# Kernel optimization log

Measured on AMD Instinct MI355X. Metric: run time of the kernel, lower is better.

Reference implementation:

```python
import jax, jax.numpy as jnp
import numpy as np

EPS = 1e-05
SCALING = 1.0


def setup_inputs() -> dict:
    key = jax.random.key(0)
    k0, k1, k2, k3, k4, k5 = jax.random.split(key, 6)
    Nx = Ny = Nz = 160          # output grid resolution per axis
    D = 48                      # factor (Kronecker) rank per axis
    W = 3                       # width0: output channels (3D flow)
    NP = 2_000_000              # query points
    K = 8                       # interpolation taps per point (trilinear)
    x = jax.random.normal(k0, (Nx, D), dtype=jnp.float32)
    y = jax.random.normal(k1, (Ny, D), dtype=jnp.float32)
    z = jax.random.normal(k2, (Nz, D), dtype=jnp.float32)
    # matches torch init: 2/sqrt(W)*rand - 1/sqrt(W)
    weight = (2.0 / np.sqrt(W)) * jax.random.uniform(k3, (W, D, D, D), dtype=jnp.float32) - (1.0 / np.sqrt(W))
    B_idx = jax.random.randint(k4, (NP, K), 0, Nx * Ny * Nz, dtype=jnp.int32)
    B_w = jax.random.uniform(k5, (NP, K), dtype=jnp.float32)
    return {"x": x, "y": y, "z": z, "weight": weight, "B_idx": B_idx, "B_w": B_w}


def reference(x, y, z, weight, B_idx, B_w):
    # Tensor-mode (Kronecker) matmuls: (W,D0,D1,D2) -> (W,Nx,Ny,Nz)
    g = jnp.einsum('ap,wpqr->waqr', x, weight)   # contract mode-0
    g = jnp.einsum('bq,waqr->wabr', y, g)        # contract mode-1
    g = jnp.einsum('cr,wabr->wabc', z, g)        # contract mode-2
    # Total-variation regularizer (isotropic, per-voxel sqrt, channel-summed)
    base = g[:, :-1, :-1, :-1]
    tv = jnp.mean(
        jnp.sqrt(
            EPS
            + (g[:, :-1, :-1, 1:] - base) ** 2
            + (g[:, :-1, 1:, :-1] - base) ** 2
            + (g[:, 1:, :-1, :-1] - base) ** 2
        ).sum(axis=0)
    )
    reg_scaled = tv * SCALING
    # Gather-weighted interpolation: flat grid (Ncells, W), K taps per point
    flat = g.reshape(g.shape[0], -1).T            # (Nx*Ny*Nz, W)
    out = (flat[B_idx] * B_w[..., None]).sum(axis=1)  # (NP, W)
    return out, reg_scaled
```

## Files before the change

### kernel.cpp

```cpp
#include <hip/hip_runtime.h>
#include <hip/hip_fp16.h>

#define D 48
#define W 3
#define NX 160
#define NY 160
#define NZ 160
#define NPTS (NX*NY*NZ)
#define KNBR 8
#define EPSV 1e-5f
#define NTV (159*159*159)
#define NBTV 2048
#define TVROWS (159*159)
#define CPAIRS 80
#define TVSLOTS (TVROWS*CPAIRS)

typedef int   vint4   __attribute__((ext_vector_type(4)));
typedef float vfloat4 __attribute__((ext_vector_type(4)));

#define T1_OFF 0
#define T1_SZ (W*NX*D*D)
#define TVP_OFF (T1_OFF + T1_SZ)
#define G3_OFF (TVP_OFF + NBTV)

__device__ inline void unpack3(uint2 u, float& f0, float& f1, float& f2) {
    __half2 lo = *reinterpret_cast<__half2*>(&u.x);
    __half2 hi = *reinterpret_cast<__half2*>(&u.y);
    f0 = __low2float(lo);
    f1 = __high2float(lo);
    f2 = __low2float(hi);
}

__global__ __launch_bounds__(256) void k1(const float* __restrict__ x,
                                          const float* __restrict__ wt,
                                          float* __restrict__ t1) {
    int lane = threadIdx.x & 63;
    int wv   = threadIdx.x >> 6;
    int q    = blockIdx.x * 4 + wv;
    int a0   = blockIdx.y * 16;
    int w    = blockIdx.z;
    bool act = lane < D;

    float wreg[D];
#pragma unroll
    for (int p = 0; p < D; ++p)
        wreg[p] = act ? wt[((w*D + p)*D + q)*D + lane] : 0.f;

    for (int ai = 0; ai < 16; ++ai) {
        int a = a0 + ai;
        const float4* xp = (const float4*)(x + a*D);
        float s = 0.f;
#pragma unroll
        for (int j = 0; j < D/4; ++j) {
            float4 xv = xp[j];
            s += xv.x * wreg[4*j+0];
            s += xv.y * wreg[4*j+1];
            s += xv.z * wreg[4*j+2];
            s += xv.w * wreg[4*j+3];
        }
        if (act) t1[((w*NX + a)*D + q)*D + lane] = s;
    }
}

#define BH 80
__global__ __launch_bounds__(192) void kbcd(const float* __restrict__ y,
                                            const float* __restrict__ z,
                                            const float* __restrict__ t1,
                                            uint2* __restrict__ g3h) {
    __shared__ float t1s[W*D*D];
    __shared__ float t2s[W*BH*D];
    int tid = threadIdx.x;
    int a   = blockIdx.y;
    int b0  = blockIdx.x * BH;

    int c = tid;
    bool act = c < NZ;
    float zreg[D];
#pragma unroll
    for (int j = 0; j < D/4; ++j) {
        float4 zv = act ? ((const float4*)(z + c*D))[j] : make_float4(0,0,0,0);
        zreg[4*j+0] = zv.x; zreg[4*j+1] = zv.y; zreg[4*j+2] = zv.z; zreg[4*j+3] = zv.w;
    }

    for (int i = tid; i < W*D*D; i += 192) {
        int w = i / (D*D), rem = i - w*(D*D);
        t1s[i] = t1[(size_t)(w*NX + a)*(D*D) + rem];
    }
    __syncthreads();

    for (int i = tid; i < W*BH*(D/4); i += 192) {
        int w   = i / (BH*(D/4));
        int rem = i - w*(BH*(D/4));
        int bh  = rem / (D/4);
        int r4  = rem - bh*(D/4);
        const float4* yb  = (const float4*)(y + (b0 + bh)*D);
        const float4* t1v = (const float4*)(t1s + w*D*D) + r4;
        float4 s = make_float4(0,0,0,0);
#pragma unroll
        for (int q4 = 0; q4 < D/4; ++q4) {
            float4 yv = yb[q4];
#pragma unroll
            for (int u = 0; u < 4; ++u) {
                float yq = (u==0) ? yv.x : (u==1) ? yv.y : (u==2) ? yv.z : yv.w;
                float4 tv = t1v[(q4*4+u)*(D/4)];
                s.x += yq*tv.x; s.y += yq*tv.y; s.z += yq*tv.z; s.w += yq*tv.w;
            }
        }
        ((float4*)t2s)[i] = s;
    }
    __syncthreads();

    for (int bh = 0; bh < BH; ++bh) {
        float acc[W];
#pragma unroll
        for (int w = 0; w < W; ++w) {
            const float4* t2v = (const float4*)(t2s + (w*BH + bh)*D);
            float s = 0.f;
#pragma unroll
            for (int j = 0; j < D/4; ++j) {
                float4 t = t2v[j];
                s += t.x*zreg[4*j+0] + t.y*zreg[4*j+1] + t.z*zreg[4*j+2] + t.w*zreg[4*j+3];
            }
            acc[w] = s;
        }
        if (act) {
            __half2 lo = __halves2half2(__float2half_rn(acc[0]), __float2half_rn(acc[1]));
            __half2 hi = __halves2half2(__float2half_rn(acc[2]), __float2half_rn(0.f));
            uint2 u;
            u.x = *reinterpret_cast<unsigned*>(&lo);
            u.y = *reinterpret_cast<unsigned*>(&hi);
            g3h[(size_t)((a*NY + (b0+bh))*NZ + c)] = u;
        }
    }
}

__device__ inline float tv3(uint2 u0, uint2 uc, uint2 ub, uint2 ua) {
    float b0,b1,b2, c0,c1,c2, d0,d1,d2, e0,e1,e2;
    unpack3(u0,b0,b1,b2); unpack3(uc,c0,c1,c2);
    unpack3(ub,d0,d1,d2); unpack3(ua,e0,e1,e2);
    float x0=c0-b0, y0=d0-b0, z0=e0-b0;
    float x1=c1-b1, y1=d1-b1, z1=e1-b1;
    float x2=c2-b2, y2=d2-b2, z2=e2-b2;
    return sqrtf(EPSV + x0*x0 + y0*y0 + z0*z0)
         + sqrtf(EPSV + x1*x1 + y1*y1 + z1*z1)
         + sqrtf(EPSV + x2*x2 + y2*y2 + z2*z2);
}

__global__ __launch_bounds__(256) void ktv(const uint2* __restrict__ g3h,
                                           float* __restrict__ partial) {
    float v = 0.f;
    for (int s = blockIdx.x * 256 + threadIdx.x; s < TVSLOTS; s += NBTV * 256) {
        int c2  = s % CPAIRS;
        int row = s / CPAIRS;
        int b   = row % 159;
        int a   = row / 159;
        int c   = 2*c2;
        size_t p = (size_t)(a*NY + b)*NZ + c;
        uint4 u0 = *(const uint4*)(g3h + p);
        uint4 ub = *(const uint4*)(g3h + p + NZ);
        uint4 ua = *(const uint4*)(g3h + p + NY*NZ);
        uint2 un = g3h[p + 2];
        uint2 u0l = make_uint2(u0.x, u0.y), u0h = make_uint2(u0.z, u0.w);
        uint2 ubl = make_uint2(ub.x, ub.y), ubh = make_uint2(ub.z, ub.w);
        uint2 ual = make_uint2(ua.x, ua.y), uah = make_uint2(ua.z, ua.w);
        v += tv3(u0l, u0h, ubl, ual);
        if (c + 1 < 159)
            v += tv3(u0h, un, ubh, uah);
    }
#pragma unroll
    for (int off = 32; off > 0; off >>= 1)
        v += __shfl_down(v, off, 64);
    __shared__ float sred[4];
    int lane = threadIdx.x & 63, wv = threadIdx.x >> 6;
    if (lane == 0) sred[wv] = v;
    __syncthreads();
    if (threadIdx.x == 0)
        partial[blockIdx.x] = sred[0] + sred[1] + sred[2] + sred[3];
}

__global__ __launch_bounds__(256) void kred(const float* __restrict__ partial,
                                            float* __restrict__ outreg) {
    float v = 0.f;
    for (int i = threadIdx.x; i < NBTV; i += 256) v += partial[i];
#pragma unroll
    for (int off = 32; off > 0; off >>= 1)
        v += __shfl_down(v, off, 64);
    __shared__ float sred[4];
    int lane = threadIdx.x & 63, wv = threadIdx.x >> 6;
    if (lane == 0) sred[wv] = v;
    __syncthreads();
    if (threadIdx.x == 0)
        outreg[0] = (sred[0] + sred[1] + sred[2] + sred[3]) * (1.0f / (float)NTV);
}

__global__ __launch_bounds__(256) void kgather(const int* __restrict__ bidx,
                                               const float* __restrict__ bw,
                                               const uint2* __restrict__ g3h,
                                               float* __restrict__ out,
                                               int np) {
    int gid  = blockIdx.x * 256 + threadIdx.x;
    int half = np >> 1;
    if (gid >= half) return;
    int n1 = gid, n2 = gid + half;

    const vint4*   ip = (const vint4*)bidx;
    const vfloat4* wp = (const vfloat4*)bw;
    vint4   i0 = __builtin_nontemporal_load(ip + (size_t)n1*2);
    vint4   i1 = __builtin_nontemporal_load(ip + (size_t)n1*2 + 1);
    vint4   j0 = __builtin_nontemporal_load(ip + (size_t)n2*2);
    vint4   j1 = __builtin_nontemporal_load(ip + (size_t)n2*2 + 1);
    vfloat4 w0 = __builtin_nontemporal_load(wp + (size_t)n1*2);
    vfloat4 w1 = __builtin_nontemporal_load(wp + (size_t)n1*2 + 1);
    vfloat4 v0 = __builtin_nontemporal_load(wp + (size_t)n2*2);
    vfloat4 v1 = __builtin_nontemporal_load(wp + (size_t)n2*2 + 1);

    int   idsA[KNBR] = {i0.x, i0.y, i0.z, i0.w, i1.x, i1.y, i1.z, i1.w};
    int   idsB[KNBR] = {j0.x, j0.y, j0.z, j0.w, j1.x, j1.y, j1.z, j1.w};
    float wwsA[KNBR] = {w0.x, w0.y, w0.z, w0.w, w1.x, w1.y, w1.z, w1.w};
    float wwsB[KNBR] = {v0.x, v0.y, v0.z, v0.w, v1.x, v1.y, v1.z, v1.w};

    uint2 uA[KNBR], uB[KNBR];
#pragma unroll
    for (int k = 0; k < KNBR; ++k) uA[k] = g3h[(size_t)idsA[k]];
#pragma unroll
    for (int k = 0; k < KNBR; ++k) uB[k] = g3h[(size_t)idsB[k]];

    float a0=0.f, a1=0.f, a2=0.f, b0=0.f, b1=0.f, b2=0.f;
#pragma unroll
    for (int k = 0; k < KNBR; ++k) {
        float f0,f1,f2;
        unpack3(uA[k], f0,f1,f2);
        a0 += f0*wwsA[k]; a1 += f1*wwsA[k]; a2 += f2*wwsA[k];
    }
#pragma unroll
    for (int k = 0; k < KNBR; ++k) {
        float f0,f1,f2;
        unpack3(uB[k], f0,f1,f2);
        b0 += f0*wwsB[k]; b1 += f1*wwsB[k]; b2 += f2*wwsB[k];
    }
    float* opA = out + (size_t)n1*3;
    float* opB = out + (size_t)n2*3;
    __builtin_nontemporal_store(a0, opA+0);
    __builtin_nontemporal_store(a1, opA+1);
    __builtin_nontemporal_store(a2, opA+2);
    __builtin_nontemporal_store(b0, opB+0);
    __builtin_nontemporal_store(b1, opB+1);
    __builtin_nontemporal_store(b2, opB+2);
}

extern "C" void kernel_launch(void* const* d_in, const int* in_sizes, int n_in,
                              void* d_out, int out_size, void* d_ws, size_t ws_size,
                              hipStream_t stream) {
    const float* x    = (const float*)d_in[0];
    const float* y    = (const float*)d_in[1];
    const float* z    = (const float*)d_in[2];
    const float* wt   = (const float*)d_in[3];
    const int*   bidx = (const int*)d_in[4];
    const float* bw   = (const float*)d_in[5];
    float* out = (float*)d_out;
    float* ws  = (float*)d_ws;

    float* t1  = ws + T1_OFF;
    float* tvp = ws + TVP_OFF;
    uint2* g3h = (uint2*)(ws + G3_OFF);
    int np = in_sizes[4] / KNBR;

    k1  <<<dim3(12, 10, 3), 256, 0, stream>>>(x, wt, t1);
    kbcd<<<dim3(2, NX),     192, 0, stream>>>(y, z, t1, g3h);

    ktv <<<dim3(NBTV), 256, 0, stream>>>(g3h, tvp);
    kred<<<dim3(1),    256, 0, stream>>>(tvp, out + (out_size - 1));

    kgather<<<dim3((np/2 + 255) / 256), 256, 0, stream>>>(bidx, bw, g3h, out, np);
}
```

Before: 524.3 us.

## Process gather taps in address slices with block sync for cache locality

The gather kernel now handles four points per thread instead of two. It walks the 4M-entry fp16 grid in 16 slices of 2^18 cells, and each thread fetches only the taps whose index falls in the current slice, with a __syncthreads between slices. The aim is to keep all blocks on the GPU working in one region of the grid at a time so the random gathers hit L2 or infinity cache more often. The cost is serialised, divergent loop passes, fewer loads in flight per thread, a barrier per slice, and fewer threads overall. Blocks are not synchronised across the whole GPU, so the locality only holds loosely.

New measurement: 1.705 ms. 3.25x slower.

```diff
diff --git a/kernel.cpp b/kernel.cpp
--- a/kernel.cpp
+++ b/kernel.cpp
@@ -14,6 +14,10 @@
 #define TVROWS (159*159)
 #define CPAIRS 80
 #define TVSLOTS (TVROWS*CPAIRS)
+
+#define SLICES 16
+#define SLICE_SHIFT 18
+#define PPT 4
 
 typedef int   vint4   __attribute__((ext_vector_type(4)));
 typedef float vfloat4 __attribute__((ext_vector_type(4)));
@@ -198,54 +202,59 @@
                                                const uint2* __restrict__ g3h,
                                                float* __restrict__ out,
                                                int np) {
-    int gid  = blockIdx.x * 256 + threadIdx.x;
-    int half = np >> 1;
-    if (gid >= half) return;
-    int n1 = gid, n2 = gid + half;
+    int gid = blockIdx.x * 256 + threadIdx.x;
+    int nth = np / PPT;
+    if (gid >= nth) return;
 
     const vint4*   ip = (const vint4*)bidx;
     const vfloat4* wp = (const vfloat4*)bw;
-    vint4   i0 = __builtin_nontemporal_load(ip + (size_t)n1*2);
-    vint4   i1 = __builtin_nontemporal_load(ip + (size_t)n1*2 + 1);
-    vint4   j0 = __builtin_nontemporal_load(ip + (size_t)n2*2);
-    vint4   j1 = __builtin_nontemporal_load(ip + (size_t)n2*2 + 1);
-    vfloat4 w0 = __builtin_nontemporal_load(wp + (size_t)n1*2);
-    vfloat4 w1 = __builtin_nontemporal_load(wp + (size_t)n1*2 + 1);
-    vfloat4 v0 = __builtin_nontemporal_load(wp + (size_t)n2*2);
-    vfloat4 v1 = __builtin_nontemporal_load(wp + (size_t)n2*2 + 1);
-
-    int   idsA[KNBR] = {i0.x, i0.y, i0.z, i0.w, i1.x, i1.y, i1.z, i1.w};
-    int   idsB[KNBR] = {j0.x, j0.y, j0.z, j0.w, j1.x, j1.y, j1.z, j1.w};
-    float wwsA[KNBR] = {w0.x, w0.y, w0.z, w0.w, w1.x, w1.y, w1.z, w1.w};
-    float wwsB[KNBR] = {v0.x, v0.y, v0.z, v0.w, v1.x, v1.y, v1.z, v1.w};
-
-    uint2 uA[KNBR], uB[KNBR];
-#pragma unroll
-    for (int k = 0; k < KNBR; ++k) uA[k] = g3h[(size_t)idsA[k]];
-#pragma unroll
-    for (int k = 0; k < KNBR; ++k) uB[k] = g3h[(size_t)idsB[k]];
-
-    float a0=0.f, a1=0.f, a2=0.f, b0=0.f, b1=0.f, b2=0.f;
-#pragma unroll
-    for (int k = 0; k < KNBR; ++k) {
-        float f0,f1,f2;
-        unpack3(uA[k], f0,f1,f2);
-        a0 += f0*wwsA[k]; a1 += f1*wwsA[k]; a2 += f2*wwsA[k];
-    }
-#pragma unroll
-    for (int k = 0; k < KNBR; ++k) {
-        float f0,f1,f2;
-        unpack3(uB[k], f0,f1,f2);
-        b0 += f0*wwsB[k]; b1 += f1*wwsB[k]; b2 += f2*wwsB[k];
-    }
-    float* opA = out + (size_t)n1*3;
-    float* opB = out + (size_t)n2*3;
-    __builtin_nontemporal_store(a0, opA+0);
-    __builtin_nontemporal_store(a1, opA+1);
-    __builtin_nontemporal_store(a2, opA+2);
-    __builtin_nontemporal_store(b0, opB+0);
-    __builtin_nontemporal_store(b1, opB+1);
-    __builtin_nontemporal_store(b2, opB+2);
+
+    int   ids[PPT*KNBR];
+    float wws[PPT*KNBR];
+#pragma unroll
+    for (int t = 0; t < PPT; ++t) {
+        size_t n = (size_t)gid + (size_t)t * nth;
+        vint4   i0 = __builtin_nontemporal_load(ip + n*2);
+        vint4   i1 = __builtin_nontemporal_load(ip + n*2 + 1);
+        vfloat4 w0 = __builtin_nontemporal_load(wp + n*2);
+        vfloat4 w1 = __builtin_nontemporal_load(wp + n*2 + 1);
+        ids[t*KNBR+0]=i0.x; ids[t*KNBR+1]=i0.y; ids[t*KNBR+2]=i0.z; ids[t*KNBR+3]=i0.w;
+        ids[t*KNBR+4]=i1.x; ids[t*KNBR+5]=i1.y; ids[t*KNBR+6]=i1.z; ids[t*KNBR+7]=i1.w;
+        wws[t*KNBR+0]=w0.x; wws[t*KNBR+1]=w0.y; wws[t*KNBR+2]=w0.z; wws[t*KNBR+3]=w0.w;
+        wws[t*KNBR+4]=w1.x; wws[t*KNBR+5]=w1.y; wws[t*KNBR+6]=w1.z; wws[t*KNBR+7]=w1.w;
+    }
+
+    float acc[PPT][3];
+#pragma unroll
+    for (int t = 0; t < PPT; ++t) { acc[t][0]=0.f; acc[t][1]=0.f; acc[t][2]=0.f; }
+
+    for (int s = 0; s < SLICES; ++s) {
+#pragma unroll
+        for (int t = 0; t < PPT; ++t) {
+#pragma unroll
+            for (int k = 0; k < KNBR; ++k) {
+                int id = ids[t*KNBR+k];
+                if ((id >> SLICE_SHIFT) == s) {
+                    uint2 u = g3h[(size_t)id];
+                    float f0,f1,f2;
+                    unpack3(u, f0,f1,f2);
+                    float wk = wws[t*KNBR+k];
+                    acc[t][0] += f0*wk;
+                    acc[t][1] += f1*wk;
+                    acc[t][2] += f2*wk;
+                }
+            }
+        }
+        __syncthreads();
+    }
+
+#pragma unroll
+    for (int t = 0; t < PPT; ++t) {
+        float* op = out + ((size_t)gid + (size_t)t * nth) * 3;
+        __builtin_nontemporal_store(acc[t][0], op+0);
+        __builtin_nontemporal_store(acc[t][1], op+1);
+        __builtin_nontemporal_store(acc[t][2], op+2);
+    }
 }
 
 extern "C" void kernel_launch(void* const* d_in, const int* in_sizes, int n_in,
@@ -271,5 +280,6 @@
     ktv <<<dim3(NBTV), 256, 0, stream>>>(g3h, tvp);
     kred<<<dim3(1),    256, 0, stream>>>(tvp, out + (out_size - 1));
 
-    kgather<<<dim3((np/2 + 255) / 256), 256, 0, stream>>>(bidx, bw, g3h, out, np);
-}
+    int nth = np / PPT;
+    kgather<<<dim3((nth + 255) / 256), 256, 0, stream>>>(bidx, bw, g3h, out, np);
+}
```
